# Kernel optimization log

Measured on AMD Instinct MI355X. Metric: run time of the kernel, lower is better.

The kernel has to match this reference:

```python
import jax, jax.numpy as jnp
import numpy as np

DIM = 256
NUM_HEADS = 8
HEAD_DIM = DIM // NUM_HEADS
SCALE = HEAD_DIM ** -0.5
KSIZE = 5


def setup_inputs() -> dict:
    key = jax.random.key(0)
    ks = jax.random.split(key, 6)
    B, C, H, W = 8, DIM, 32, 32
    x = jax.random.normal(ks[0], (B, C, H, W), dtype=jnp.float32)
    qkv_w = jax.random.normal(ks[1], (3 * C, C), dtype=jnp.float32) * 0.02  # 1x1 conv, no bias
    proj_w = jax.random.normal(ks[2], (C, C), dtype=jnp.float32) * 0.02    # 1x1 conv
    proj_b = jax.random.normal(ks[3], (C,), dtype=jnp.float32) * 0.02
    lepe_w = jax.random.normal(ks[4], (C, 1, KSIZE, KSIZE), dtype=jnp.float32) * 0.02  # depthwise
    lepe_b = jax.random.normal(ks[5], (C,), dtype=jnp.float32) * 0.02
    return {"x": x, "qkv_w": qkv_w, "proj_w": proj_w, "proj_b": proj_b,
            "lepe_w": lepe_w, "lepe_b": lepe_b}


def _forward(x, qkv_w, proj_w, proj_b, lepe_w, lepe_b):
    B, C, H, W = x.shape
    N = H * W
    # 1x1 conv qkv: [B,3C,H,W]
    qkv = jnp.einsum('bchw,oc->bohw', x, qkv_w)
    q, k, v = jnp.split(qkv, 3, axis=1)
    # reshape to [B, heads, head_dim, N]
    qh = q.reshape(B, NUM_HEADS, HEAD_DIM, N)
    kh = k.reshape(B, NUM_HEADS, HEAD_DIM, N)
    vh = v.reshape(B, NUM_HEADS, HEAD_DIM, N)
    # attn = (q^T k) * scale, softmax over keys -> [B, heads, N, N]
    attn = jnp.einsum('bhdn,bhdm->bhnm', qh, kh)
    attn = jax.nn.softmax(attn * SCALE, axis=-1)
    # out = attn @ v^T -> [B, heads, N, head_dim] -> [B, C, H, W]
    out = jnp.einsum('bhnm,bhdm->bhdn', attn, vh).reshape(B, C, H, W)
    # LePE: depthwise conv on v (image layout) + residual add
    lepe = jax.lax.conv_general_dilated(
        v, lepe_w, window_strides=(1, 1),
        padding=[(KSIZE // 2, KSIZE // 2)] * 2,
        dimension_numbers=('NCHW', 'OIHW', 'NCHW'),
        feature_group_count=C) + lepe_b[None, :, None, None]
    out = out + lepe
    # 1x1 proj
    out = jnp.einsum('bchw,oc->bohw', out, proj_w) + proj_b[None, :, None, None]
    return out


def reference(x, qkv_w, proj_w, proj_b, lepe_w, lepe_b):
    return _forward(x, qkv_w, proj_w, proj_b, lepe_w, lepe_b)
```

## Files before the change

### kernel.cpp

```cpp
#include <hip/hip_runtime.h>

#define NB 8
#define NC 256
#define NN 1024

typedef unsigned short u16;
typedef unsigned int u32;
typedef __attribute__((ext_vector_type(8))) short short8;
typedef __attribute__((ext_vector_type(4))) float f32x4;

__device__ __forceinline__ u16 f2b(float f){ union{float ff;u32 i;}v; v.ff=f; u32 r=v.i+0x7FFFu+((v.i>>16)&1u); return (u16)(r>>16); }
__device__ __forceinline__ float b2f(u16 p){ union{u32 i;float f;}v; v.i=((u32)p)<<16; return v.f; }
__device__ __forceinline__ float pklo(u32 p){ union{u32 i;float f;}v; v.i=p<<16; return v.f; }
__device__ __forceinline__ float pkhi(u32 p){ union{u32 i;float f;}v; v.i=p&0xFFFF0000u; return v.f; }

#define QSC 0.25503486f

union FR { uint4 u; short8 s; };

__global__ void __launch_bounds__(256) k_cast(const float* __restrict__ x,
                                              u16* __restrict__ xt){
  const int n0 = blockIdx.x*64, c0 = blockIdx.y*128, b = blockIdx.z;
  const int tid = threadIdx.x;
  __shared__ u16 lt[64][136];
  #pragma unroll
  for (int cc = 0; cc < 4; cc++){
    const int c = c0 + cc*32 + (tid>>3);
    const int ns = (tid&7)*8;
    const float* src = x + ((size_t)(b*NC + c))*NN + n0 + ns;
    float4 a = *(const float4*)src;
    float4 d = *(const float4*)(src+4);
    const int cl = c - c0;
    lt[ns+0][cl] = f2b(a.x); lt[ns+1][cl] = f2b(a.y);
    lt[ns+2][cl] = f2b(a.z); lt[ns+3][cl] = f2b(a.w);
    lt[ns+4][cl] = f2b(d.x); lt[ns+5][cl] = f2b(d.y);
    lt[ns+6][cl] = f2b(d.z); lt[ns+7][cl] = f2b(d.w);
  }
  __syncthreads();
  #pragma unroll
  for (int p = 0; p < 4; p++){
    const int flat = p*256 + tid;
    const int row = flat >> 4, seg = flat & 15;
    uint4 d = *(uint4*)&lt[row][seg*8];
    *(uint4*)(xt + ((size_t)(b*NN + n0 + row))*NC + c0 + seg*8) = d;
  }
}

__global__ void __launch_bounds__(256) k_qkv(const float* __restrict__ wq,
                                             const u16* __restrict__ xt,
                                             u16* __restrict__ qt,
                                             u16* __restrict__ kt,
                                             u16* __restrict__ v){
  const int ot = blockIdx.x >> 5, nb = blockIdx.x & 31;
  const int nt = nb >> 3, b = nb & 7;
  const int o0 = ot*32;
  const int tid = threadIdx.x, wv = tid>>6, lane = tid&63;
  const int l15 = lane&15, quad = lane>>4;
  const int n0w = nt*256 + wv*64;
  __shared__ u16 swq[32][264];
  __shared__ u16 s2[4][64][40];
  #pragma unroll
  for (int i = 0; i < 8; i++){
    const int flat = i*256 + tid;
    const int row = flat >> 6, c4 = flat & 63;
    float4 a = *(const float4*)(wq + (size_t)(o0+row)*NC + c4*4);
    uint2 p;
    p.x = (u32)f2b(a.x) | ((u32)f2b(a.y)<<16);
    p.y = (u32)f2b(a.z) | ((u32)f2b(a.w)<<16);
    *(uint2*)&swq[row][c4*4] = p;
  }
  __syncthreads();
  f32x4 acc[2][4];
  #pragma unroll
  for (int mt = 0; mt < 2; mt++)
    #pragma unroll
    for (int nt2 = 0; nt2 < 4; nt2++) acc[mt][nt2] = (f32x4){0.f,0.f,0.f,0.f};
  const u16* xb = xt + ((size_t)(b*NN + n0w))*NC;
  for (int k0 = 0; k0 < 256; k0 += 32){
    FR af[2], bf[4];
    af[0].u = *(uint4*)&swq[l15][k0 + quad*8];
    af[1].u = *(uint4*)&swq[16+l15][k0 + quad*8];
    #pragma unroll
    for (int nt2 = 0; nt2 < 4; nt2++)
      bf[nt2].u = *(const uint4*)(xb + (size_t)(nt2*16+l15)*NC + k0 + quad*8);
    #pragma unroll
    for (int mt = 0; mt < 2; mt++)
      #pragma unroll
      for (int nt2 = 0; nt2 < 4; nt2++)
        acc[mt][nt2] = __builtin_amdgcn_mfma_f32_16x16x32_bf16(af[mt].s, bf[nt2].s, acc[mt][nt2], 0,0,0);
  }
  if (ot < 16){
    const float sc = (ot < 8) ? QSC : 1.0f;
    u16* dstbase = (ot < 8) ? qt : kt;
    const int h = (ot < 8) ? ot : ot-8;
    #pragma unroll
    for (int mt = 0; mt < 2; mt++)
      #pragma unroll
      for (int nt2 = 0; nt2 < 4; nt2++){
        uint2 w;
        w.x = (u32)f2b(acc[mt][nt2][0]*sc) | ((u32)f2b(acc[mt][nt2][1]*sc)<<16);
        w.y = (u32)f2b(acc[mt][nt2][2]*sc) | ((u32)f2b(acc[mt][nt2][3]*sc)<<16);
        *(uint2*)&s2[wv][nt2*16+l15][mt*16+quad*4] = w;
      }
    __syncthreads();
    u16* db = dstbase + ((size_t)(b*8+h)*NN + n0w)*32;
    #pragma unroll
    for (int p = 0; p < 4; p++){
      const int n_loc = p*16 + (lane>>2), seg = lane&3;
      uint4 d = *(uint4*)&s2[wv][n_loc][seg*8];
      *(uint4*)(db + (size_t)n_loc*32 + seg*8) = d;
    }
  } else {
    const int c0 = o0 - 512;
    #pragma unroll
    for (int mt = 0; mt < 2; mt++)
      #pragma unroll
      for (int nt2 = 0; nt2 < 4; nt2++)
        #pragma unroll
        for (int r = 0; r < 4; r++)
          v[(size_t)(b*NC + c0 + mt*16 + quad*4 + r)*NN + n0w + nt2*16 + l15] = f2b(acc[mt][nt2][r]);
  }
}

__global__ void __launch_bounds__(256) k_attn(const u16* __restrict__ qt,
                                              const u16* __restrict__ kt,
                                              const u16* __restrict__ v,
                                              const float* __restrict__ lw,
                                              const float* __restrict__ lb,
                                              u16* __restrict__ tt){
  const int cq = blockIdx.x >> 6, bh = blockIdx.x & 63;
  const int b = bh >> 3, h = bh & 7;
  const int tid = threadIdx.x;
  const int wv = tid >> 6, lane = tid & 63;
  const int l15 = lane & 15, quad = lane >> 4;
  const int q0 = (cq*4 + wv)*32;

  __shared__ u16 pb[4][2][2][16][40];
  __shared__ u16 vstage[8][32][38];
  __shared__ u16 s_out[4][32][36];

  {
    const int rr = tid >> 5, lc2 = tid & 31;
    const int yy = cq*4 - 2 + rr;
    u32* dst32 = (u32*)&vstage[rr][lc2][0];
    if (yy < 0 || yy > 31){
      #pragma unroll
      for (int j = 0; j < 19; j++) dst32[j] = 0;
    } else {
      const u16* src = v + ((size_t)(b*NC + h*32 + lc2))*NN + yy*32;
      uint4 a = *(const uint4*)src;
      uint4 b4 = *(const uint4*)(src+8);
      uint4 c4 = *(const uint4*)(src+16);
      uint4 d4 = *(const uint4*)(src+24);
      dst32[0] = 0;
      dst32[1]=a.x;  dst32[2]=a.y;  dst32[3]=a.z;  dst32[4]=a.w;
      dst32[5]=b4.x; dst32[6]=b4.y; dst32[7]=b4.z; dst32[8]=b4.w;
      dst32[9]=c4.x; dst32[10]=c4.y; dst32[11]=c4.z; dst32[12]=c4.w;
      dst32[13]=d4.x; dst32[14]=d4.y; dst32[15]=d4.z; dst32[16]=d4.w;
      dst32[17]=0; dst32[18]=0;
    }
  }
  __syncthreads();

  const u16* qtb = qt + (size_t)bh*NN*32;
  const u16* ktb = kt + (size_t)bh*NN*32;
  const u16* vbp = v + (size_t)(b*256 + h*32)*NN;

  FR qa, qb_;
  qa.u  = *(const uint4*)(qtb + (size_t)(q0      + l15)*32 + quad*8);
  qb_.u = *(const uint4*)(qtb + (size_t)(q0 + 16 + l15)*32 + quad*8);

  f32x4 z = {0.f,0.f,0.f,0.f};
  f32x4 oA0 = z, oA1 = z, oB0 = z, oB1 = z;
  float denA[4] = {0.f,0.f,0.f,0.f}, denB[4] = {0.f,0.f,0.f,0.f};

  FR kc0, kc1, vc0, vc1;
  kc0.u = *(const uint4*)(ktb + (size_t)(l15     )*32 + quad*8);
  kc1.u = *(const uint4*)(ktb + (size_t)(16 + l15)*32 + quad*8);
  vc0.u = *(const uint4*)(vbp + (size_t)(l15     )*NN + quad*8);
  vc1.u = *(const uint4*)(vbp + (size_t)(16 + l15)*NN + quad*8);

  {
    f32x4 sA0 = __builtin_amdgcn_mfma_f32_16x16x32_bf16(qa.s,  kc0.s, z, 0,0,0);
    f32x4 sA1 = __builtin_amdgcn_mfma_f32_16x16x32_bf16(qa.s,  kc1.s, z, 0,0,0);
    f32x4 sB0 = __builtin_amdgcn_mfma_f32_16x16x32_bf16(qb_.s, kc0.s, z, 0,0,0);
    f32x4 sB1 = __builtin_amdgcn_mfma_f32_16x16x32_bf16(qb_.s, kc1.s, z, 0,0,0);
    u16* pA = &pb[wv][0][0][0][0];
    u16* pB = &pb[wv][0][1][0][0];
    #pragma unroll
    for (int r = 0; r < 4; r++){
      float pA0 = __builtin_amdgcn_exp2f(sA0[r]);
      float pA1 = __builtin_amdgcn_exp2f(sA1[r]);
      float pB0 = __builtin_amdgcn_exp2f(sB0[r]);
      float pB1 = __builtin_amdgcn_exp2f(sB1[r]);
      denA[r] += pA0 + pA1;
      denB[r] += pB0 + pB1;
      const int row = (quad*4 + r)*40;
      pA[row + l15]      = (u16)(__float_as_uint(pA0)>>16);
      pA[row + 16 + l15] = (u16)(__float_as_uint(pA1)>>16);
      pB[row + l15]      = (u16)(__float_as_uint(pB0)>>16);
      pB[row + 16 + l15] = (u16)(__float_as_uint(pB1)>>16);
    }
  }

  for (int it = 1; it < 32; it++){
    const int m0 = it*32;
    FR kn0, kn1, vn0, vn1;
    kn0.u = *(const uint4*)(ktb + (size_t)(m0      + l15)*32 + quad*8);
    kn1.u = *(const uint4*)(ktb + (size_t)(m0 + 16 + l15)*32 + quad*8);
    vn0.u = *(const uint4*)(vbp + (size_t)(l15     )*NN + m0 + quad*8);
    vn1.u = *(const uint4*)(vbp + (size_t)(16 + l15)*NN + m0 + quad*8);

    {
      const u16* pbr = &pb[wv][(it-1)&1][0][0][0];
      FR pfA, pfB;
      pfA.u = *(const uint4*)(pbr + l15*40 + quad*8);
      pfB.u = *(const uint4*)(pbr + 640 + l15*40 + quad*8);
      oA0 = __builtin_amdgcn_mfma_f32_16x16x32_bf16(pfA.s, vc0.s, oA0, 0,0,0);
      oA1 = __builtin_amdgcn_mfma_f32_16x16x32_bf16(pfA.s, vc1.s, oA1, 0,0,0);
      oB0 = __builtin_amdgcn_mfma_f32_16x16x32_bf16(pfB.s, vc0.s, oB0, 0,0,0);
      oB1 = __builtin_amdgcn_mfma_f32_16x16x32_bf16(pfB.s, vc1.s, oB1, 0,0,0);
    }
    {
      f32x4 sA0 = __builtin_amdgcn_mfma_f32_16x16x32_bf16(qa.s,  kn0.s, z, 0,0,0);
      f32x4 sA1 = __builtin_amdgcn_mfma_f32_16x16x32_bf16(qa.s,  kn1.s, z, 0,0,0);
      f32x4 sB0 = __builtin_amdgcn_mfma_f32_16x16x32_bf16(qb_.s, kn0.s, z, 0,0,0);
      f32x4 sB1 = __builtin_amdgcn_mfma_f32_16x16x32_bf16(qb_.s, kn1.s, z, 0,0,0);
      u16* pA = &pb[wv][it&1][0][0][0];
      u16* pB = &pb[wv][it&1][1][0][0];
      #pragma unroll
      for (int r = 0; r < 4; r++){
        float pA0 = __builtin_amdgcn_exp2f(sA0[r]);
        float pA1 = __builtin_amdgcn_exp2f(sA1[r]);
        float pB0 = __builtin_amdgcn_exp2f(sB0[r]);
        float pB1 = __builtin_amdgcn_exp2f(sB1[r]);
        denA[r] += pA0 + pA1;
        denB[r] += pB0 + pB1;
        const int row = (quad*4 + r)*40;
        pA[row + l15]      = (u16)(__float_as_uint(pA0)>>16);
        pA[row + 16 + l15] = (u16)(__float_as_uint(pA1)>>16);
        pB[row + l15]      = (u16)(__float_as_uint(pB0)>>16);
        pB[row + 16 + l15] = (u16)(__float_as_uint(pB1)>>16);
      }
    }
    kc0 = kn0; kc1 = kn1; vc0 = vn0; vc1 = vn1;
  }
  {
    const u16* pbr = &pb[wv][1][0][0][0];
    FR pfA, pfB;
    pfA.u = *(const uint4*)(pbr + l15*40 + quad*8);
    pfB.u = *(const uint4*)(pbr + 640 + l15*40 + quad*8);
    oA0 = __builtin_amdgcn_mfma_f32_16x16x32_bf16(pfA.s, vc0.s, oA0, 0,0,0);
    oA1 = __builtin_amdgcn_mfma_f32_16x16x32_bf16(pfA.s, vc1.s, oA1, 0,0,0);
    oB0 = __builtin_amdgcn_mfma_f32_16x16x32_bf16(pfB.s, vc0.s, oB0, 0,0,0);
    oB1 = __builtin_amdgcn_mfma_f32_16x16x32_bf16(pfB.s, vc1.s, oB1, 0,0,0);
  }

  #pragma unroll
  for (int r = 0; r < 4; r++){
    #pragma unroll
    for (int m = 1; m < 16; m <<= 1){
      denA[r] += __shfl_xor(denA[r], m);
      denB[r] += __shfl_xor(denB[r], m);
    }
  }
  {
    u16* so = &s_out[wv][0][0];
    #pragma unroll
    for (int r = 0; r < 4; r++){
      const int q = quad*4 + r;
      const float iA = 1.f/denA[r], iB = 1.f/denB[r];
      so[q*36 + l15]           = f2b(oA0[r]*iA);
      so[q*36 + 16 + l15]      = f2b(oA1[r]*iA);
      so[(q+16)*36 + l15]      = f2b(oB0[r]*iB);
      so[(q+16)*36 + 16 + l15] = f2b(oB1[r]*iB);
    }
  }
  {
    const int lc = lane & 31, qh = lane >> 5;
    float lep[16];
    const float lbias = lb[h*32 + lc];
    #pragma unroll
    for (int i = 0; i < 16; i++) lep[i] = lbias;
    const float* lwc = lw + (size_t)(h*32 + lc)*25;
    #pragma unroll
    for (int ky = 0; ky < 5; ky++){
      const u32* vr = (const u32*)&vstage[wv + ky][lc][0];
      float vv[20];
      #pragma unroll
      for (int jj = 0; jj < 10; jj++){
        u32 pk = vr[qh*8 + jj];
        vv[2*jj]   = pklo(pk);
        vv[2*jj+1] = pkhi(pk);
      }
      const float w0 = lwc[ky*5+0], w1 = lwc[ky*5+1], w2 = lwc[ky*5+2],
                  w3 = lwc[ky*5+3], w4 = lwc[ky*5+4];
      #pragma unroll
      for (int i = 0; i < 16; i++)
        lep[i] += w0*vv[i] + w1*vv[i+1] + w2*vv[i+2] + w3*vv[i+3] + w4*vv[i+4];
    }
    u16* tb = tt + ((size_t)(b*NN + q0))*NC + h*32;
    const u16* so = &s_out[wv][0][0];
    #pragma unroll
    for (int i = 0; i < 16; i++){
      const int q = qh*16 + i;
      tb[(size_t)q*NC + lc] = f2b(b2f(so[q*36 + lc]) + lep[i]);
    }
  }
}

__global__ void __launch_bounds__(256) k_proj(const float* __restrict__ wp,
                                              const u16* __restrict__ tt,
                                              const float* __restrict__ pbias,
                                              float* __restrict__ out){
  const int ot = blockIdx.x >> 6, rest = blockIdx.x & 63;
  const int nt = rest >> 3, b = rest & 7;
  const int o0 = ot*32;
  const int tid = threadIdx.x, wv = tid>>6, lane = tid&63;
  const int l15 = lane&15, quad = lane>>4;
  const int n0w = nt*128 + wv*32;
  __shared__ u16 swp[32][264];
  #pragma unroll
  for (int i = 0; i < 8; i++){
    const int flat = i*256 + tid;
    const int row = flat >> 6, c4 = flat & 63;
    float4 a = *(const float4*)(wp + (size_t)(o0+row)*NC + c4*4);
    uint2 p;
    p.x = (u32)f2b(a.x) | ((u32)f2b(a.y)<<16);
    p.y = (u32)f2b(a.z) | ((u32)f2b(a.w)<<16);
    *(uint2*)&swp[row][c4*4] = p;
  }
  __syncthreads();
  f32x4 acc[2][2];
  #pragma unroll
  for (int mt = 0; mt < 2; mt++)
    #pragma unroll
    for (int n2 = 0; n2 < 2; n2++) acc[mt][n2] = (f32x4){0.f,0.f,0.f,0.f};
  const u16* tb = tt + ((size_t)(b*NN + n0w))*NC;
  for (int k0 = 0; k0 < 256; k0 += 32){
    FR af[2], bf[2];
    af[0].u = *(uint4*)&swp[l15][k0 + quad*8];
    af[1].u = *(uint4*)&swp[16+l15][k0 + quad*8];
    bf[0].u = *(const uint4*)(tb + (size_t)(l15     )*NC + k0 + quad*8);
    bf[1].u = *(const uint4*)(tb + (size_t)(16 + l15)*NC + k0 + quad*8);
    #pragma unroll
    for (int mt = 0; mt < 2; mt++)
      #pragma unroll
      for (int n2 = 0; n2 < 2; n2++)
        acc[mt][n2] = __builtin_amdgcn_mfma_f32_16x16x32_bf16(af[mt].s, bf[n2].s, acc[mt][n2], 0,0,0);
  }
  float bv[2][4];
  #pragma unroll
  for (int mt = 0; mt < 2; mt++)
    #pragma unroll
    for (int r = 0; r < 4; r++) bv[mt][r] = pbias[o0 + mt*16 + quad*4 + r];
  #pragma unroll
  for (int mt = 0; mt < 2; mt++)
    #pragma unroll
    for (int n2 = 0; n2 < 2; n2++)
      #pragma unroll
      for (int r = 0; r < 4; r++)
        out[(size_t)(b*NC + o0 + mt*16 + quad*4 + r)*NN + n0w + n2*16 + l15] = acc[mt][n2][r] + bv[mt][r];
}

extern "C" void kernel_launch(void* const* d_in, const int* in_sizes, int n_in,
                              void* d_out, int out_size, void* d_ws, size_t ws_size,
                              hipStream_t stream){
  const float* x      = (const float*)d_in[0];
  const float* qkv_w  = (const float*)d_in[1];
  const float* proj_w = (const float*)d_in[2];
  const float* proj_b = (const float*)d_in[3];
  const float* lepe_w = (const float*)d_in[4];
  const float* lepe_b = (const float*)d_in[5];
  float* out = (float*)d_out;

  if (ws_size < (size_t)20*1024*1024) return;
  u16* xt = (u16*)d_ws;
  u16* qt = xt + 2097152;
  u16* kt = qt + 2097152;
  u16* v  = kt + 2097152;
  u16* tt = v  + 2097152;

  k_cast<<<dim3(16, 2, 8), 256, 0, stream>>>(x, xt);
  k_qkv <<<dim3(768),      256, 0, stream>>>(qkv_w, xt, qt, kt, v);
  k_attn<<<dim3(512),      256, 0, stream>>>(qt, kt, v, lepe_w, lepe_b, tt);
  k_proj<<<dim3(512),      256, 0, stream>>>(proj_w, tt, proj_b, out);
}
```

Baseline: 123.0 us.

## Split attention key range across warps and retile QKV GEMM to 64x128

```diff
diff --git a/kernel.cpp b/kernel.cpp
--- a/kernel.cpp
+++ b/kernel.cpp
@@ -51,16 +51,16 @@
                                              u16* __restrict__ qt,
                                              u16* __restrict__ kt,
                                              u16* __restrict__ v){
-  const int ot = blockIdx.x >> 5, nb = blockIdx.x & 31;
-  const int nt = nb >> 3, b = nb & 7;
-  const int o0 = ot*32;
+  const int ot = blockIdx.x >> 6, rest = blockIdx.x & 63;
+  const int nt = rest >> 3, b = rest & 7;
+  const int o0 = ot*64;
   const int tid = threadIdx.x, wv = tid>>6, lane = tid&63;
   const int l15 = lane&15, quad = lane>>4;
-  const int n0w = nt*256 + wv*64;
-  __shared__ u16 swq[32][264];
-  __shared__ u16 s2[4][64][40];
-  #pragma unroll
-  for (int i = 0; i < 8; i++){
+  const int n0w = nt*128 + wv*32;
+  __shared__ u16 swq[64][264];
+  __shared__ u16 s2[4][32][72];
+  #pragma unroll
+  for (int i = 0; i < 16; i++){
     const int flat = i*256 + tid;
     const int row = flat >> 6, c4 = flat & 63;
     float4 a = *(const float4*)(wq + (size_t)(o0+row)*NC + c4*4);
@@ -70,94 +70,102 @@
     *(uint2*)&swq[row][c4*4] = p;
   }
   __syncthreads();
-  f32x4 acc[2][4];
-  #pragma unroll
-  for (int mt = 0; mt < 2; mt++)
-    #pragma unroll
-    for (int nt2 = 0; nt2 < 4; nt2++) acc[mt][nt2] = (f32x4){0.f,0.f,0.f,0.f};
+  f32x4 acc[4][2];
+  #pragma unroll
+  for (int mt = 0; mt < 4; mt++)
+    #pragma unroll
+    for (int n2 = 0; n2 < 2; n2++) acc[mt][n2] = (f32x4){0.f,0.f,0.f,0.f};
   const u16* xb = xt + ((size_t)(b*NN + n0w))*NC;
   for (int k0 = 0; k0 < 256; k0 += 32){
-    FR af[2], bf[4];
-    af[0].u = *(uint4*)&swq[l15][k0 + quad*8];
-    af[1].u = *(uint4*)&swq[16+l15][k0 + quad*8];
-    #pragma unroll
-    for (int nt2 = 0; nt2 < 4; nt2++)
-      bf[nt2].u = *(const uint4*)(xb + (size_t)(nt2*16+l15)*NC + k0 + quad*8);
-    #pragma unroll
-    for (int mt = 0; mt < 2; mt++)
-      #pragma unroll
-      for (int nt2 = 0; nt2 < 4; nt2++)
-        acc[mt][nt2] = __builtin_amdgcn_mfma_f32_16x16x32_bf16(af[mt].s, bf[nt2].s, acc[mt][nt2], 0,0,0);
-  }
-  if (ot < 16){
-    const float sc = (ot < 8) ? QSC : 1.0f;
-    u16* dstbase = (ot < 8) ? qt : kt;
-    const int h = (ot < 8) ? ot : ot-8;
-    #pragma unroll
-    for (int mt = 0; mt < 2; mt++)
-      #pragma unroll
-      for (int nt2 = 0; nt2 < 4; nt2++){
+    FR af[4], bf[2];
+    #pragma unroll
+    for (int mt = 0; mt < 4; mt++)
+      af[mt].u = *(uint4*)&swq[mt*16 + l15][k0 + quad*8];
+    #pragma unroll
+    for (int n2 = 0; n2 < 2; n2++)
+      bf[n2].u = *(const uint4*)(xb + (size_t)(n2*16+l15)*NC + k0 + quad*8);
+    #pragma unroll
+    for (int mt = 0; mt < 4; mt++)
+      #pragma unroll
+      for (int n2 = 0; n2 < 2; n2++)
+        acc[mt][n2] = __builtin_amdgcn_mfma_f32_16x16x32_bf16(af[mt].s, bf[n2].s, acc[mt][n2], 0,0,0);
+  }
+  if (ot < 8){
+    const float sc = (ot < 4) ? QSC : 1.0f;
+    u16* dstbase = (ot < 4) ? qt : kt;
+    const int h0 = (ot < 4) ? (o0 >> 5) : ((o0-256) >> 5);
+    #pragma unroll
+    for (int mt = 0; mt < 4; mt++)
+      #pragma unroll
+      for (int n2 = 0; n2 < 2; n2++){
         uint2 w;
-        w.x = (u32)f2b(acc[mt][nt2][0]*sc) | ((u32)f2b(acc[mt][nt2][1]*sc)<<16);
-        w.y = (u32)f2b(acc[mt][nt2][2]*sc) | ((u32)f2b(acc[mt][nt2][3]*sc)<<16);
-        *(uint2*)&s2[wv][nt2*16+l15][mt*16+quad*4] = w;
+        w.x = (u32)f2b(acc[mt][n2][0]*sc) | ((u32)f2b(acc[mt][n2][1]*sc)<<16);
+        w.y = (u32)f2b(acc[mt][n2][2]*sc) | ((u32)f2b(acc[mt][n2][3]*sc)<<16);
+        *(uint2*)&s2[wv][n2*16+l15][mt*16+quad*4] = w;
       }
     __syncthreads();
-    u16* db = dstbase + ((size_t)(b*8+h)*NN + n0w)*32;
     #pragma unroll
     for (int p = 0; p < 4; p++){
-      const int n_loc = p*16 + (lane>>2), seg = lane&3;
-      uint4 d = *(uint4*)&s2[wv][n_loc][seg*8];
-      *(uint4*)(db + (size_t)n_loc*32 + seg*8) = d;
+      const int u = p*64 + lane;
+      const int hh = u >> 7, rem = u & 127;
+      const int n_loc = rem >> 2, seg = rem & 3;
+      uint4 d = *(uint4*)&s2[wv][n_loc][hh*32 + seg*8];
+      u16* db = dstbase + ((size_t)(b*8 + h0 + hh)*NN + n0w + n_loc)*32 + seg*8;
+      *(uint4*)db = d;
     }
   } else {
     const int c0 = o0 - 512;
     #pragma unroll
-    for (int mt = 0; mt < 2; mt++)
-      #pragma unroll
-      for (int nt2 = 0; nt2 < 4; nt2++)
+    for (int mt = 0; mt < 4; mt++)
+      #pragma unroll
+      for (int n2 = 0; n2 < 2; n2++)
         #pragma unroll
         for (int r = 0; r < 4; r++)
-          v[(size_t)(b*NC + c0 + mt*16 + quad*4 + r)*NN + n0w + nt2*16 + l15] = f2b(acc[mt][nt2][r]);
-  }
-}
-
-__global__ void __launch_bounds__(256) k_attn(const u16* __restrict__ qt,
-                                              const u16* __restrict__ kt,
-                                              const u16* __restrict__ v,
-                                              const float* __restrict__ lw,
-                                              const float* __restrict__ lb,
-                                              u16* __restrict__ tt){
-  const int cq = blockIdx.x >> 6, bh = blockIdx.x & 63;
+          v[(size_t)(b*NC + c0 + mt*16 + quad*4 + r)*NN + n0w + n2*16 + l15] = f2b(acc[mt][n2][r]);
+  }
+}
+
+__global__ void __launch_bounds__(256, 4) k_attn(const u16* __restrict__ qt,
+                                                 const u16* __restrict__ kt,
+                                                 const u16* __restrict__ v,
+                                                 const float* __restrict__ lw,
+                                                 const float* __restrict__ lb,
+                                                 u16* __restrict__ tt){
+  const int qt2 = blockIdx.x >> 6, bh = blockIdx.x & 63;
   const int b = bh >> 3, h = bh & 7;
   const int tid = threadIdx.x;
   const int wv = tid >> 6, lane = tid & 63;
   const int l15 = lane & 15, quad = lane >> 4;
-  const int q0 = (cq*4 + wv)*32;
-
-  __shared__ u16 pb[4][2][2][16][40];
-  __shared__ u16 vstage[8][32][38];
-  __shared__ u16 s_out[4][32][36];
+  const int qg = wv & 1, kh = wv >> 1;
+  const int q0 = qt2*64 + qg*32;
+
+  __shared__ u16 pb[4][2][16][40];
+  __shared__ u16 vstage[6][32][38];
+  __shared__ u16 s_out[2][32][36];
+  __shared__ float mnum[2][32][33];
+  __shared__ float mden[2][32];
 
   {
     const int rr = tid >> 5, lc2 = tid & 31;
-    const int yy = cq*4 - 2 + rr;
-    u32* dst32 = (u32*)&vstage[rr][lc2][0];
-    if (yy < 0 || yy > 31){
-      #pragma unroll
-      for (int j = 0; j < 19; j++) dst32[j] = 0;
-    } else {
-      const u16* src = v + ((size_t)(b*NC + h*32 + lc2))*NN + yy*32;
-      uint4 a = *(const uint4*)src;
-      uint4 b4 = *(const uint4*)(src+8);
-      uint4 c4 = *(const uint4*)(src+16);
-      uint4 d4 = *(const uint4*)(src+24);
-      dst32[0] = 0;
-      dst32[1]=a.x;  dst32[2]=a.y;  dst32[3]=a.z;  dst32[4]=a.w;
-      dst32[5]=b4.x; dst32[6]=b4.y; dst32[7]=b4.z; dst32[8]=b4.w;
-      dst32[9]=c4.x; dst32[10]=c4.y; dst32[11]=c4.z; dst32[12]=c4.w;
-      dst32[13]=d4.x; dst32[14]=d4.y; dst32[15]=d4.z; dst32[16]=d4.w;
-      dst32[17]=0; dst32[18]=0;
+    if (rr < 6){
+      const int yy = qt2*2 - 2 + rr;
+      u32* dst32 = (u32*)&vstage[rr][lc2][0];
+      if (yy < 0 || yy > 31){
+        #pragma unroll
+        for (int j = 0; j < 19; j++) dst32[j] = 0;
+      } else {
+        const u16* src = v + ((size_t)(b*NC + h*32 + lc2))*NN + yy*32;
+        uint4 a = *(const uint4*)src;
+        uint4 b4 = *(const uint4*)(src+8);
+        uint4 c4 = *(const uint4*)(src+16);
+        uint4 d4 = *(const uint4*)(src+24);
+        dst32[0] = 0;
+        dst32[1]=a.x;  dst32[2]=a.y;  dst32[3]=a.z;  dst32[4]=a.w;
+        dst32[5]=b4.x; dst32[6]=b4.y; dst32[7]=b4.z; dst32[8]=b4.w;
+        dst32[9]=c4.x; dst32[10]=c4.y; dst32[11]=c4.z; dst32[12]=c4.w;
+        dst32[13]=d4.x; dst32[14]=d4.y; dst32[15]=d4.z; dst32[16]=d4.w;
+        dst32[17]=0; dst32[18]=0;
+      }
     }
   }
   __syncthreads();
@@ -174,19 +182,22 @@
   f32x4 oA0 = z, oA1 = z, oB0 = z, oB1 = z;
   float denA[4] = {0.f,0.f,0.f,0.f}, denB[4] = {0.f,0.f,0.f,0.f};
 
-  FR kc0, kc1, vc0, vc1;
-  kc0.u = *(const uint4*)(ktb + (size_t)(l15     )*32 + quad*8);
-  kc1.u = *(const uint4*)(ktb + (size_t)(16 + l15)*32 + quad*8);
-  vc0.u = *(const uint4*)(vbp + (size_t)(l15     )*NN + quad*8);
-  vc1.u = *(const uint4*)(vbp + (size_t)(16 + l15)*NN + quad*8);
-
-  {
-    f32x4 sA0 = __builtin_amdgcn_mfma_f32_16x16x32_bf16(qa.s,  kc0.s, z, 0,0,0);
-    f32x4 sA1 = __builtin_amdgcn_mfma_f32_16x16x32_bf16(qa.s,  kc1.s, z, 0,0,0);
-    f32x4 sB0 = __builtin_amdgcn_mfma_f32_16x16x32_bf16(qb_.s, kc0.s, z, 0,0,0);
-    f32x4 sB1 = __builtin_amdgcn_mfma_f32_16x16x32_bf16(qb_.s, kc1.s, z, 0,0,0);
-    u16* pA = &pb[wv][0][0][0][0];
-    u16* pB = &pb[wv][0][1][0][0];
+  u16* pA = &pb[wv][0][0][0];
+  u16* pB = &pb[wv][1][0][0];
+
+  for (int it = 0; it < 16; it++){
+    const int m0 = kh*512 + it*32;
+    FR kf0, kf1, vf0, vf1;
+    kf0.u = *(const uint4*)(ktb + (size_t)(m0      + l15)*32 + quad*8);
+    kf1.u = *(const uint4*)(ktb + (size_t)(m0 + 16 + l15)*32 + quad*8);
+    vf0.u = *(const uint4*)(vbp + (size_t)(l15     )*NN + m0 + quad*8);
+    vf1.u = *(const uint4*)(vbp + (size_t)(16 + l15)*NN + m0 + quad*8);
+
+    f32x4 sA0 = __builtin_amdgcn_mfma_f32_16x16x32_bf16(qa.s,  kf0.s, z, 0,0,0);
+    f32x4 sA1 = __builtin_amdgcn_mfma_f32_16x16x32_bf16(qa.s,  kf1.s, z, 0,0,0);
+    f32x4 sB0 = __builtin_amdgcn_mfma_f32_16x16x32_bf16(qb_.s, kf0.s, z, 0,0,0);
+    f32x4 sB1 = __builtin_amdgcn_mfma_f32_16x16x32_bf16(qb_.s, kf1.s, z, 0,0,0);
+
     #pragma unroll
     for (int r = 0; r < 4; r++){
       float pA0 = __builtin_amdgcn_exp2f(sA0[r]);
@@ -201,61 +212,15 @@
       pB[row + l15]      = (u16)(__float_as_uint(pB0)>>16);
       pB[row + 16 + l15] = (u16)(__float_as_uint(pB1)>>16);
     }
-  }
-
-  for (int it = 1; it < 32; it++){
-    const int m0 = it*32;
-    FR kn0, kn1, vn0, vn1;
-    kn0.u = *(const uint4*)(ktb + (size_t)(m0      + l15)*32 + quad*8);
-    kn1.u = *(const uint4*)(ktb + (size_t)(m0 + 16 + l15)*32 + quad*8);
-    vn0.u = *(const uint4*)(vbp + (size_t)(l15     )*NN + m0 + quad*8);
-    vn1.u = *(const uint4*)(vbp + (size_t)(16 + l15)*NN + m0 + quad*8);
-
-    {
-      const u16* pbr = &pb[wv][(it-1)&1][0][0][0];
-      FR pfA, pfB;
-      pfA.u = *(const uint4*)(pbr + l15*40 + quad*8);
-      pfB.u = *(const uint4*)(pbr + 640 + l15*40 + quad*8);
-      oA0 = __builtin_amdgcn_mfma_f32_16x16x32_bf16(pfA.s, vc0.s, oA0, 0,0,0);
-      oA1 = __builtin_amdgcn_mfma_f32_16x16x32_bf16(pfA.s, vc1.s, oA1, 0,0,0);
-      oB0 = __builtin_amdgcn_mfma_f32_16x16x32_bf16(pfB.s, vc0.s, oB0, 0,0,0);
-      oB1 = __builtin_amdgcn_mfma_f32_16x16x32_bf16(pfB.s, vc1.s, oB1, 0,0,0);
-    }
-    {
-      f32x4 sA0 = __builtin_amdgcn_mfma_f32_16x16x32_bf16(qa.s,  kn0.s, z, 0,0,0);
-      f32x4 sA1 = __builtin_amdgcn_mfma_f32_16x16x32_bf16(qa.s,  kn1.s, z, 0,0,0);
-      f32x4 sB0 = __builtin_amdgcn_mfma_f32_16x16x32_bf16(qb_.s, kn0.s, z, 0,0,0);
-      f32x4 sB1 = __builtin_amdgcn_mfma_f32_16x16x32_bf16(qb_.s, kn1.s, z, 0,0,0);
-      u16* pA = &pb[wv][it&1][0][0][0];
-      u16* pB = &pb[wv][it&1][1][0][0];
-      #pragma unroll
-      for (int r = 0; r < 4; r++){
-        float pA0 = __builtin_amdgcn_exp2f(sA0[r]);
-        float pA1 = __builtin_amdgcn_exp2f(sA1[r]);
-        float pB0 = __builtin_amdgcn_exp2f(sB0[r]);
-        float pB1 = __builtin_amdgcn_exp2f(sB1[r]);
-        denA[r] += pA0 + pA1;
-        denB[r] += pB0 + pB1;
-        const int row = (quad*4 + r)*40;
-        pA[row + l15]      = (u16)(__float_as_uint(pA0)>>16);
-        pA[row + 16 + l15] = (u16)(__float_as_uint(pA1)>>16);
-        pB[row + l15]      = (u16)(__float_as_uint(pB0)>>16);
-        pB[row + 16 + l15] = (u16)(__float_as_uint(pB1)>>16);
-      }
-    }
-    kc0 = kn0; kc1 = kn1; vc0 = vn0; vc1 = vn1;
-  }
-  {
-    const u16* pbr = &pb[wv][1][0][0][0];
     FR pfA, pfB;
-    pfA.u = *(const uint4*)(pbr + l15*40 + quad*8);
-    pfB.u = *(const uint4*)(pbr + 640 + l15*40 + quad*8);
-    oA0 = __builtin_amdgcn_mfma_f32_16x16x32_bf16(pfA.s, vc0.s, oA0, 0,0,0);
-    oA1 = __builtin_amdgcn_mfma_f32_16x16x32_bf16(pfA.s, vc1.s, oA1, 0,0,0);
-    oB0 = __builtin_amdgcn_mfma_f32_16x16x32_bf16(pfB.s, vc0.s, oB0, 0,0,0);
-    oB1 = __builtin_amdgcn_mfma_f32_16x16x32_bf16(pfB.s, vc1.s, oB1, 0,0,0);
-  }
-
+    pfA.u = *(const uint4*)(pA + l15*40 + quad*8);
+    pfB.u = *(const uint4*)(pB + l15*40 + quad*8);
+
+    oA0 = __builtin_amdgcn_mfma_f32_16x16x32_bf16(pfA.s, vf0.s, oA0, 0,0,0);
+    oA1 = __builtin_amdgcn_mfma_f32_16x16x32_bf16(pfA.s, vf1.s, oA1, 0,0,0);
+    oB0 = __builtin_amdgcn_mfma_f32_16x16x32_bf16(pfB.s, vf0.s, oB0, 0,0,0);
+    oB1 = __builtin_amdgcn_mfma_f32_16x16x32_bf16(pfB.s, vf1.s, oB1, 0,0,0);
+  }
   #pragma unroll
   for (int r = 0; r < 4; r++){
     #pragma unroll
@@ -264,19 +229,37 @@
       denB[r] += __shfl_xor(denB[r], m);
     }
   }
-  {
-    u16* so = &s_out[wv][0][0];
+  __syncthreads();
+  if (kh == 1){
+    #pragma unroll
+    for (int r = 0; r < 4; r++){
+      mnum[qg][quad*4 + r][l15]          = oA0[r];
+      mnum[qg][quad*4 + r][16 + l15]     = oA1[r];
+      mnum[qg][16 + quad*4 + r][l15]     = oB0[r];
+      mnum[qg][16 + quad*4 + r][16 + l15]= oB1[r];
+    }
+    if (l15 == 0){
+      #pragma unroll
+      for (int r = 0; r < 4; r++){
+        mden[qg][quad*4 + r]      = denA[r];
+        mden[qg][16 + quad*4 + r] = denB[r];
+      }
+    }
+  }
+  __syncthreads();
+  if (kh == 0){
+    u16* so = &s_out[qg][0][0];
     #pragma unroll
     for (int r = 0; r < 4; r++){
       const int q = quad*4 + r;
-      const float iA = 1.f/denA[r], iB = 1.f/denB[r];
-      so[q*36 + l15]           = f2b(oA0[r]*iA);
-      so[q*36 + 16 + l15]      = f2b(oA1[r]*iA);
-      so[(q+16)*36 + l15]      = f2b(oB0[r]*iB);
-      so[(q+16)*36 + 16 + l15] = f2b(oB1[r]*iB);
-    }
-  }
-  {
+      const float dA = denA[r] + mden[qg][q];
+      const float dB = denB[r] + mden[qg][16 + q];
+      const float iA = 1.f/dA, iB = 1.f/dB;
+      so[q*36 + l15]           = f2b((oA0[r] + mnum[qg][q][l15])*iA);
+      so[q*36 + 16 + l15]      = f2b((oA1[r] + mnum[qg][q][16+l15])*iA);
+      so[(q+16)*36 + l15]      = f2b((oB0[r] + mnum[qg][16+q][l15])*iB);
+      so[(q+16)*36 + 16 + l15] = f2b((oB1[r] + mnum[qg][16+q][16+l15])*iB);
+    }
     const int lc = lane & 31, qh = lane >> 5;
     float lep[16];
     const float lbias = lb[h*32 + lc];
@@ -285,7 +268,7 @@
     const float* lwc = lw + (size_t)(h*32 + lc)*25;
     #pragma unroll
     for (int ky = 0; ky < 5; ky++){
-      const u32* vr = (const u32*)&vstage[wv + ky][lc][0];
+      const u32* vr = (const u32*)&vstage[qg + ky][lc][0];
       float vv[20];
       #pragma unroll
       for (int jj = 0; jj < 10; jj++){
@@ -300,7 +283,6 @@
         lep[i] += w0*vv[i] + w1*vv[i+1] + w2*vv[i+2] + w3*vv[i+3] + w4*vv[i+4];
     }
     u16* tb = tt + ((size_t)(b*NN + q0))*NC + h*32;
-    const u16* so = &s_out[wv][0][0];
     #pragma unroll
     for (int i = 0; i < 16; i++){
       const int q = qh*16 + i;
@@ -383,6 +365,6 @@
 
   k_cast<<<dim3(16, 2, 8), 256, 0, stream>>>(x, xt);
   k_qkv <<<dim3(768),      256, 0, stream>>>(qkv_w, xt, qt, kt, v);
-  k_attn<<<dim3(512),      256, 0, stream>>>(qt, kt, v, lepe_w, lepe_b, tt);
+  k_attn<<<dim3(1024),     256, 0, stream>>>(qt, kt, v, lepe_w, lepe_b, tt);
   k_proj<<<dim3(512),      256, 0, stream>>>(proj_w, tt, proj_b, out);
 }
```

Result: no change. 123.0 us, median of 2 (+0.1%).
